# Kernel optimization log

Hardware: AMD Instinct MI355X
Metric: run time of the kernel (lower is better)

## Reference

```python
import jax, jax.numpy as jnp
import numpy as np

NUM_CLUSTERS = 256
NUM_HEADS = 16
DIM_PER_HEAD = 64
NGRAM_VOCAB = 768 * 256
NGRAM_EMB_DIM = 8
DECAY = 0.999
EPS_PQ = 1e-06
LN_EPS = 1e-05


def _first_primes_after(start, count):
    primes = []
    n = start
    while len(primes) < count:
        n += 1
        if all(n % p for p in range(2, int(n ** 0.5) + 1)):
            primes.append(n)
    return np.array(primes, dtype=np.int64)

# first NUM_HEADS primes in (NGRAM_VOCAB, 2*NGRAM_VOCAB), matching sympy.primerange
_PRIMES = _first_primes_after(NGRAM_VOCAB, NUM_HEADS)


def _layer_norm(v, scale, bias):
    # reduction over last axis; per-(head, feature) scale/bias (flax feature_axes=(-2,-1))
    mu = jnp.mean(v, axis=-1, keepdims=True)
    var = jnp.var(v, axis=-1, keepdims=True)
    return (v - mu) * jax.lax.rsqrt(var + LN_EPS) * scale + bias


def setup_inputs() -> dict:
    key = jax.random.key(0)
    k1, k2, k3 = jax.random.split(key, 3)
    B, L = 4, 4096
    x = jax.random.normal(k1, (B, L, NUM_HEADS * DIM_PER_HEAD), dtype=jnp.float32)
    means = jax.random.normal(k2, (NUM_HEADS, NUM_CLUSTERS, DIM_PER_HEAD), dtype=jnp.float32)
    embed_table = jax.random.normal(k3, (NGRAM_VOCAB * NUM_HEADS, NGRAM_EMB_DIM), dtype=jnp.float32)
    ln_x_scale = jnp.ones((NUM_HEADS, DIM_PER_HEAD), dtype=jnp.float32)
    ln_x_bias = jnp.zeros((NUM_HEADS, DIM_PER_HEAD), dtype=jnp.float32)
    ln_y_scale = jnp.ones((NUM_HEADS, NGRAM_EMB_DIM), dtype=jnp.float32)
    ln_y_bias = jnp.zeros((NUM_HEADS, NGRAM_EMB_DIM), dtype=jnp.float32)
    return {"x": x, "means": means, "embed_table": embed_table,
            "ln_x_scale": ln_x_scale, "ln_x_bias": ln_x_bias,
            "ln_y_scale": ln_y_scale, "ln_y_bias": ln_y_bias}


def reference(x, means, embed_table, ln_x_scale, ln_x_bias, ln_y_scale, ln_y_bias):
    B, L, HD = x.shape
    H, K, D = means.shape
    E = NGRAM_EMB_DIM
    xh = x.reshape(B, L, H, D)

    # --- ProductQuantization: squared-distance cluster assignment ---
    x_sq = jnp.sum(jnp.square(xh), axis=-1, keepdims=True)            # [B,L,H,1]
    m_sq = jnp.sum(jnp.square(means), axis=-1)[None, None]            # [1,1,H,K]
    dists = x_sq + m_sq - 2.0 * jnp.einsum('blhd,hkd->blhk', xh, means)
    cluster_ids = jnp.argmin(dists, axis=-1).astype(jnp.int32)        # [B,L,H]

    # --- EMA means update (train-mode side effect) ---
    one_hot = jax.nn.one_hot(cluster_ids, K, dtype=xh.dtype)          # [B,L,H,K]
    counts = jnp.sum(one_hot, axis=(0, 1))                            # [H,K]
    sum_x = jnp.einsum('blhk,blhd->hkd', one_hot, xh)                 # [H,K,D]
    means_x = sum_x / (EPS_PQ + counts[..., None])
    new_means = (1.0 - DECAY) * means_x + DECAY * means

    # --- bigram ids: ids[t] + ids[t-1] * vocab ---
    prev = jnp.pad(cluster_ids[:, :-1], ((0, 0), (1, 0), (0, 0)))     # [B,L,H]
    ngram_cluster_ids = cluster_ids + prev * NUM_CLUSTERS             # < K*K, fits int32

    # --- multi-way hash per head ---
    head = jnp.arange(H, dtype=jnp.int32)                             # [H]
    primes = jnp.asarray(_PRIMES, dtype=jnp.int32)                    # [H]
    hashed = (ngram_cluster_ids * (head + 1) + (head + 1)) % primes % NGRAM_VOCAB
    ngram_ids = hashed + NGRAM_VOCAB * head                           # [B,L,H]

    # --- ngram embedding gather + per-head LayerNorms + concat ---
    y = embed_table[ngram_ids]                                        # [B,L,H,E]
    normed_x = _layer_norm(xh, ln_x_scale, ln_x_bias)
    normed_y = _layer_norm(y, ln_y_scale, ln_y_bias)
    out = jnp.concatenate((normed_x[..., : D - E], normed_y), axis=-1)
    out = out.reshape(B, L, H * D)
    return out, new_means
```

## Files before the change

kernel.cpp:

```cpp
#include <hip/hip_runtime.h>
#include <cstdint>
#include <cstddef>

#define NH 16
#define ND 64
#define NK 256
#define NE 8
#define NV 196608
#define NBL 16384
#define TOK 64
#define MROW 17
#define ACC_STRIDE 257

struct Primes { int p[NH]; };

__global__ __launch_bounds__(512, 4) void k_pq(
    const float* __restrict__ x, const float* __restrict__ means,
    const float* __restrict__ lnxs, const float* __restrict__ lnxb,
    float* __restrict__ out, uint8_t* __restrict__ cids,
    float* __restrict__ gsum, int* __restrict__ gcnt)
{
  __shared__ __align__(16) float smem[18176];
  float4* sm4   = (float4*)smem;
  float*  smsq2 = smem + 17408;
  int*    scnt  = (int*)(smem + 17920);
  float*  accum = smem;

  const int tid = threadIdx.x;
  const int c   = tid & 31;
  const int r   = tid >> 5;
  const int h   = blockIdx.y;
  const int g0  = blockIdx.x * TOK;

  {
    const int cl = tid & 255, hf = tid >> 8;
    const float4* src = (const float4*)(means + ((size_t)h * NK + cl) * ND + hf * 32);
    float mp = 0.f;
#pragma unroll
    for (int i = 0; i < 8; ++i) {
      float4 v = src[i];
      sm4[cl * MROW + hf * 8 + i] = v;
      mp += v.x * v.x + v.y * v.y + v.z * v.z + v.w * v.w;
    }
    smsq2[hf * NK + cl] = mp;
    if (tid < NK) scnt[tid] = 0;
  }
  __syncthreads();

  float acc[4][8];
#pragma unroll
  for (int j = 0; j < 4; ++j)
#pragma unroll
    for (int i = 0; i < 8; ++i) acc[j][i] = 0.f;

  const float* xb = x + ((size_t)(g0 + r * 4) * NH + h) * ND;

#pragma unroll 2
  for (int dc = 0; dc < 16; ++dc) {
    float4 xv[4];
#pragma unroll
    for (int j = 0; j < 4; ++j)
      xv[j] = *(const float4*)(xb + j * (NH * ND) + dc * 4);
#pragma unroll
    for (int i = 0; i < 8; ++i) {
      float4 mv = sm4[(i * 32 + c) * MROW + dc];
#pragma unroll
      for (int j = 0; j < 4; ++j) {
        float a = acc[j][i];
        a = fmaf(xv[j].x, mv.x, a);
        a = fmaf(xv[j].y, mv.y, a);
        a = fmaf(xv[j].z, mv.z, a);
        a = fmaf(xv[j].w, mv.w, a);
        acc[j][i] = a;
      }
    }
  }

  int bk[4];
  {
    float bv[4]; int bi_[4];
#pragma unroll
    for (int j = 0; j < 4; ++j) { bv[j] = 3.4e38f; bi_[j] = 0; }
#pragma unroll
    for (int i = 0; i < 8; ++i) {
      const int cl = i * 32 + c;
      const float mq = smsq2[cl] + smsq2[NK + cl];
#pragma unroll
      for (int j = 0; j < 4; ++j) {
        float d = mq - 2.0f * acc[j][i];
        if (d < bv[j]) { bv[j] = d; bi_[j] = cl; }
      }
    }
#pragma unroll
    for (int j = 0; j < 4; ++j) {
      float v = bv[j]; int id = bi_[j];
#pragma unroll
      for (int m = 1; m < 32; m <<= 1) {
        float ov = __shfl_xor(v, m);
        int   oi = __shfl_xor(id, m);
        if (ov < v || (ov == v && oi < id)) { v = ov; id = oi; }
      }
      bk[j] = id;
    }
    if (c == 0) {
#pragma unroll
      for (int j = 0; j < 4; ++j) {
        cids[(size_t)(g0 + r * 4 + j) * NH + h] = (uint8_t)bk[j];
        atomicAdd(&scnt[bk[j]], 1);
      }
    }
  }

  __syncthreads();
  for (int idx = tid; idx < ND * ACC_STRIDE; idx += 512) accum[idx] = 0.f;
  __syncthreads();

#pragma unroll
  for (int j = 0; j < 4; ++j) {
    const float* xt = x + ((size_t)(g0 + r * 4 + j) * NH + h) * ND + c * 2;
    float2 v = *(const float2*)xt;
    atomicAdd(&accum[(c * 2 + 0) * ACC_STRIDE + bk[j]], v.x);
    atomicAdd(&accum[(c * 2 + 1) * ACC_STRIDE + bk[j]], v.y);
  }

  {
    const int tl = tid >> 4, q = tid & 15;
#pragma unroll
    for (int rep = 0; rep < 2; ++rep) {
      const int t = tl + rep * 32;
      float4 v = *(const float4*)(x + ((size_t)(g0 + t) * NH + h) * ND + q * 4);
      float s  = v.x + v.y + v.z + v.w;
      float sq = v.x * v.x + v.y * v.y + v.z * v.z + v.w * v.w;
#pragma unroll
      for (int m = 1; m < 16; m <<= 1) { s += __shfl_xor(s, m); sq += __shfl_xor(sq, m); }
      float mu  = s * (1.f / 64.f);
      float var = sq * (1.f / 64.f) - mu * mu;
      float rs  = rsqrtf(var + 1e-5f);
      if (q < 14) {
        float4 sc = *(const float4*)(lnxs + h * ND + q * 4);
        float4 bi = *(const float4*)(lnxb + h * ND + q * 4);
        float4 o;
        o.x = (v.x - mu) * rs * sc.x + bi.x;
        o.y = (v.y - mu) * rs * sc.y + bi.y;
        o.z = (v.z - mu) * rs * sc.z + bi.z;
        o.w = (v.w - mu) * rs * sc.w + bi.w;
        *(float4*)(out + ((size_t)(g0 + t) * NH + h) * ND + q * 4) = o;
      }
    }
  }
  __syncthreads();

  {
    const int cl = tid & 255, dh = tid >> 8;
    const int cnt = scnt[cl];
    if (cnt > 0) {
      if (dh == 0) atomicAdd(&gcnt[h * NK + cl], cnt);
#pragma unroll 4
      for (int d = dh * 32; d < dh * 32 + 32; ++d)
        atomicAdd(&gsum[((size_t)h * ND + d) * NK + cl], accum[d * ACC_STRIDE + cl]);
    }
  }
}

__global__ __launch_bounds__(256) void k_ngram(
    const uint8_t* __restrict__ cids, const float* __restrict__ embed,
    const float* __restrict__ lys, const float* __restrict__ lyb,
    float* __restrict__ out, Primes pr)
{
  const int i = blockIdx.x * 256 + threadIdx.x;
  const int h = i & 15;
  const int g = i >> 4;
  const int l = g & 4095;

  int cid  = (int)cids[i];
  int prev = (l == 0) ? 0 : (int)cids[i - NH];
  int ng   = cid + (prev << 8);
  int hp1  = h + 1;
  int v    = ng * hp1 + hp1;
  const int p = pr.p[h];
  while (v >= p) v -= p;
  if (v >= NV) v -= NV;

  const float4* e4 = (const float4*)(embed + ((size_t)(v + NV * h)) * NE);
  float4 y0 = e4[0], y1 = e4[1];

  float s = ((y0.x + y0.y) + (y0.z + y0.w)) + ((y1.x + y1.y) + (y1.z + y1.w));
  float mu = s * 0.125f;
  float q = y0.x * y0.x + y0.y * y0.y + y0.z * y0.z + y0.w * y0.w
          + y1.x * y1.x + y1.y * y1.y + y1.z * y1.z + y1.w * y1.w;
  float var = q * 0.125f - mu * mu;
  float rs  = rsqrtf(var + 1e-5f);

  const float* sc = lys + h * NE;
  const float* bi = lyb + h * NE;
  float4 o0, o1;
  o0.x = (y0.x - mu) * rs * sc[0] + bi[0];
  o0.y = (y0.y - mu) * rs * sc[1] + bi[1];
  o0.z = (y0.z - mu) * rs * sc[2] + bi[2];
  o0.w = (y0.w - mu) * rs * sc[3] + bi[3];
  o1.x = (y1.x - mu) * rs * sc[4] + bi[4];
  o1.y = (y1.y - mu) * rs * sc[5] + bi[5];
  o1.z = (y1.z - mu) * rs * sc[6] + bi[6];
  o1.w = (y1.w - mu) * rs * sc[7] + bi[7];

  float4* orow = (float4*)(out + ((size_t)g * NH + h) * ND + 56);
  orow[0] = o0;
  orow[1] = o1;
}

__global__ __launch_bounds__(256) void k_means(
    const float* __restrict__ means, const float* __restrict__ gsum,
    const int* __restrict__ gcnt, float* __restrict__ newm)
{
  const int i = blockIdx.x * 256 + threadIdx.x;
  const int d = i & 63;
  const int k = (i >> 6) & 255;
  const int h = i >> 14;
  float cnt = (float)gcnt[h * NK + k];
  float sx  = gsum[((size_t)h * ND + d) * NK + k];
  float mx  = sx / (1e-6f + cnt);
  newm[i] = 0.001f * mx + 0.999f * means[i];
}

extern "C" void kernel_launch(void* const* d_in, const int* in_sizes, int n_in,
                              void* d_out, int out_size, void* d_ws, size_t ws_size,
                              hipStream_t stream)
{
  const float* x     = (const float*)d_in[0];
  const float* means = (const float*)d_in[1];
  const float* embed = (const float*)d_in[2];
  const float* lnxs  = (const float*)d_in[3];
  const float* lnxb  = (const float*)d_in[4];
  const float* lys   = (const float*)d_in[5];
  const float* lyb   = (const float*)d_in[6];

  float* out  = (float*)d_out;
  float* newm = out + (size_t)NBL * NH * ND;

  float*   gsum = (float*)d_ws;
  int*     gcnt = (int*)((char*)d_ws + (size_t)NH * NK * ND * 4);
  uint8_t* cids = (uint8_t*)((char*)d_ws + (size_t)NH * NK * ND * 4 + (size_t)NH * NK * 4);

  hipMemsetAsync(d_ws, 0, (size_t)NH * NK * ND * 4 + (size_t)NH * NK * 4, stream);

  Primes pr;
  {
    int n = NV, c = 0;
    while (c < NH) {
      ++n;
      bool isp = true;
      for (int q = 2; (long long)q * q <= n; ++q)
        if (n % q == 0) { isp = false; break; }
      if (isp) pr.p[c++] = n;
    }
  }

  dim3 g1(NBL / TOK, NH);
  k_pq<<<g1, 512, 0, stream>>>(x, means, lnxs, lnxb, out, cids, gsum, gcnt);
  k_ngram<<<(NBL * NH) / 256, 256, 0, stream>>>(cids, embed, lys, lyb, out, pr);
  k_means<<<(NH * NK * ND) / 256, 256, 0, stream>>>(means, gsum, gcnt, newm);
}
```

Baseline: 336.7 us.

## Double tokens per PQ block, relayout global sums, widen LayerNorm per thread

Each PQ block now handles 128 tokens instead of 64, with every thread computing 8 tokens × 8 clusters. This reuses each shared-memory means load across more FMAs and halves the number of global atomic flushes for sums and counts. The global sum buffer moves to an [h][k][d] layout so the flush atomics write contiguous d addresses and the means-update kernel reads it linearly. The x LayerNorm now gives each thread 16 elements with fewer shuffles. The larger accumulator tile raises register pressure and halves the grid, which may reduce occupancy.

```diff
diff --git a/kernel.cpp b/kernel.cpp
--- a/kernel.cpp
+++ b/kernel.cpp
@@ -8,7 +8,7 @@
 #define NE 8
 #define NV 196608
 #define NBL 16384
-#define TOK 64
+#define TOK 128
 #define MROW 17
 #define ACC_STRIDE 257
 
@@ -47,25 +47,25 @@
   }
   __syncthreads();
 
-  float acc[4][8];
-#pragma unroll
-  for (int j = 0; j < 4; ++j)
+  float acc[8][8];
+#pragma unroll
+  for (int j = 0; j < 8; ++j)
 #pragma unroll
     for (int i = 0; i < 8; ++i) acc[j][i] = 0.f;
 
-  const float* xb = x + ((size_t)(g0 + r * 4) * NH + h) * ND;
+  const float* xb = x + ((size_t)(g0 + r * 8) * NH + h) * ND;
 
 #pragma unroll 2
   for (int dc = 0; dc < 16; ++dc) {
-    float4 xv[4];
-#pragma unroll
-    for (int j = 0; j < 4; ++j)
-      xv[j] = *(const float4*)(xb + j * (NH * ND) + dc * 4);
+    float4 xv[8];
+#pragma unroll
+    for (int j = 0; j < 8; ++j)
+      xv[j] = *(const float4*)(xb + (size_t)j * (NH * ND) + dc * 4);
 #pragma unroll
     for (int i = 0; i < 8; ++i) {
       float4 mv = sm4[(i * 32 + c) * MROW + dc];
 #pragma unroll
-      for (int j = 0; j < 4; ++j) {
+      for (int j = 0; j < 8; ++j) {
         float a = acc[j][i];
         a = fmaf(xv[j].x, mv.x, a);
         a = fmaf(xv[j].y, mv.y, a);
@@ -76,23 +76,23 @@
     }
   }
 
-  int bk[4];
-  {
-    float bv[4]; int bi_[4];
-#pragma unroll
-    for (int j = 0; j < 4; ++j) { bv[j] = 3.4e38f; bi_[j] = 0; }
+  int bk[8];
+  {
+    float bv[8]; int bi_[8];
+#pragma unroll
+    for (int j = 0; j < 8; ++j) { bv[j] = 3.4e38f; bi_[j] = 0; }
 #pragma unroll
     for (int i = 0; i < 8; ++i) {
       const int cl = i * 32 + c;
       const float mq = smsq2[cl] + smsq2[NK + cl];
 #pragma unroll
-      for (int j = 0; j < 4; ++j) {
+      for (int j = 0; j < 8; ++j) {
         float d = mq - 2.0f * acc[j][i];
         if (d < bv[j]) { bv[j] = d; bi_[j] = cl; }
       }
     }
 #pragma unroll
-    for (int j = 0; j < 4; ++j) {
+    for (int j = 0; j < 8; ++j) {
       float v = bv[j]; int id = bi_[j];
 #pragma unroll
       for (int m = 1; m < 32; m <<= 1) {
@@ -104,8 +104,8 @@
     }
     if (c == 0) {
 #pragma unroll
-      for (int j = 0; j < 4; ++j) {
-        cids[(size_t)(g0 + r * 4 + j) * NH + h] = (uint8_t)bk[j];
+      for (int j = 0; j < 8; ++j) {
+        cids[(size_t)(g0 + r * 8 + j) * NH + h] = (uint8_t)bk[j];
         atomicAdd(&scnt[bk[j]], 1);
       }
     }
@@ -116,49 +116,53 @@
   __syncthreads();
 
 #pragma unroll
-  for (int j = 0; j < 4; ++j) {
-    const float* xt = x + ((size_t)(g0 + r * 4 + j) * NH + h) * ND + c * 2;
-    float2 v = *(const float2*)xt;
+  for (int j = 0; j < 8; ++j) {
+    float2 v = *(const float2*)(x + ((size_t)(g0 + r * 8 + j) * NH + h) * ND + c * 2);
     atomicAdd(&accum[(c * 2 + 0) * ACC_STRIDE + bk[j]], v.x);
     atomicAdd(&accum[(c * 2 + 1) * ACC_STRIDE + bk[j]], v.y);
   }
 
   {
-    const int tl = tid >> 4, q = tid & 15;
-#pragma unroll
-    for (int rep = 0; rep < 2; ++rep) {
-      const int t = tl + rep * 32;
-      float4 v = *(const float4*)(x + ((size_t)(g0 + t) * NH + h) * ND + q * 4);
-      float s  = v.x + v.y + v.z + v.w;
-      float sq = v.x * v.x + v.y * v.y + v.z * v.z + v.w * v.w;
-#pragma unroll
-      for (int m = 1; m < 16; m <<= 1) { s += __shfl_xor(s, m); sq += __shfl_xor(sq, m); }
-      float mu  = s * (1.f / 64.f);
-      float var = sq * (1.f / 64.f) - mu * mu;
-      float rs  = rsqrtf(var + 1e-5f);
-      if (q < 14) {
-        float4 sc = *(const float4*)(lnxs + h * ND + q * 4);
-        float4 bi = *(const float4*)(lnxb + h * ND + q * 4);
+    const int tl = tid >> 2, q = tid & 3;
+    const float* xt = x + ((size_t)(g0 + tl) * NH + h) * ND + q * 16;
+    float4 v[4];
+    float s = 0.f, sq = 0.f;
+#pragma unroll
+    for (int j = 0; j < 4; ++j) {
+      v[j] = *(const float4*)(xt + j * 4);
+      s  += v[j].x + v[j].y + v[j].z + v[j].w;
+      sq += v[j].x * v[j].x + v[j].y * v[j].y + v[j].z * v[j].z + v[j].w * v[j].w;
+    }
+    s  += __shfl_xor(s, 1);  sq += __shfl_xor(sq, 1);
+    s  += __shfl_xor(s, 2);  sq += __shfl_xor(sq, 2);
+    float mu  = s * (1.f / 64.f);
+    float var = sq * (1.f / 64.f) - mu * mu;
+    float rs  = rsqrtf(var + 1e-5f);
+    float* orow = out + ((size_t)(g0 + tl) * NH + h) * ND + q * 16;
+#pragma unroll
+    for (int j = 0; j < 4; ++j) {
+      const int d = q * 16 + j * 4;
+      if (d < 56) {
+        float4 sc = *(const float4*)(lnxs + h * ND + d);
+        float4 bi = *(const float4*)(lnxb + h * ND + d);
         float4 o;
-        o.x = (v.x - mu) * rs * sc.x + bi.x;
-        o.y = (v.y - mu) * rs * sc.y + bi.y;
-        o.z = (v.z - mu) * rs * sc.z + bi.z;
-        o.w = (v.w - mu) * rs * sc.w + bi.w;
-        *(float4*)(out + ((size_t)(g0 + t) * NH + h) * ND + q * 4) = o;
-      }
-    }
-  }
-  __syncthreads();
-
-  {
-    const int cl = tid & 255, dh = tid >> 8;
-    const int cnt = scnt[cl];
-    if (cnt > 0) {
-      if (dh == 0) atomicAdd(&gcnt[h * NK + cl], cnt);
-#pragma unroll 4
-      for (int d = dh * 32; d < dh * 32 + 32; ++d)
-        atomicAdd(&gsum[((size_t)h * ND + d) * NK + cl], accum[d * ACC_STRIDE + cl]);
-    }
+        o.x = (v[j].x - mu) * rs * sc.x + bi.x;
+        o.y = (v[j].y - mu) * rs * sc.y + bi.y;
+        o.z = (v[j].z - mu) * rs * sc.z + bi.z;
+        o.w = (v[j].w - mu) * rs * sc.w + bi.w;
+        *(float4*)(orow + j * 4) = o;
+      }
+    }
+  }
+  __syncthreads();
+
+  {
+    const int d = tid & 63, grp = tid >> 6;
+    for (int cl = grp; cl < NK; cl += 8) {
+      if (scnt[cl] > 0)
+        atomicAdd(&gsum[(((size_t)h << 8) + cl) * ND + d], accum[d * ACC_STRIDE + cl]);
+    }
+    if (tid < NK && scnt[tid] > 0) atomicAdd(&gcnt[h * NK + tid], scnt[tid]);
   }
 }
 
@@ -213,12 +217,8 @@
     const int* __restrict__ gcnt, float* __restrict__ newm)
 {
   const int i = blockIdx.x * 256 + threadIdx.x;
-  const int d = i & 63;
-  const int k = (i >> 6) & 255;
-  const int h = i >> 14;
-  float cnt = (float)gcnt[h * NK + k];
-  float sx  = gsum[((size_t)h * ND + d) * NK + k];
-  float mx  = sx / (1e-6f + cnt);
+  float cnt = (float)gcnt[i >> 6];
+  float mx  = gsum[i] / (1e-6f + cnt);
   newm[i] = 0.001f * mx + 0.999f * means[i];
 }
 
```

Result: slower. 450.2 us (+33.7%).

## Compact active clusters, coalesce global sum atomics, prefetch x in PQ kernel

Applied to the files above, without the earlier changes.

Builds a compacted list of clusters that received tokens, then flushes per-cluster sums with one thread per dimension. The global sum buffer changes to [H,K,D] layout so the atomics are contiguous and the means kernel indexes it directly. This replaces the old scattered atomic loop that ran once per cluster over all 256 clusters. It also software-prefetches the next x chunk in the distance loop, reshapes the x LayerNorm to 8 lanes per token, and relaxes launch bounds to 2 waves, which may raise register use at the cost of occupancy.

```diff
diff --git a/kernel.cpp b/kernel.cpp
--- a/kernel.cpp
+++ b/kernel.cpp
@@ -14,17 +14,19 @@
 
 struct Primes { int p[NH]; };
 
-__global__ __launch_bounds__(512, 4) void k_pq(
+__global__ __launch_bounds__(512, 2) void k_pq(
     const float* __restrict__ x, const float* __restrict__ means,
     const float* __restrict__ lnxs, const float* __restrict__ lnxb,
     float* __restrict__ out, uint8_t* __restrict__ cids,
     float* __restrict__ gsum, int* __restrict__ gcnt)
 {
-  __shared__ __align__(16) float smem[18176];
-  float4* sm4   = (float4*)smem;
-  float*  smsq2 = smem + 17408;
-  int*    scnt  = (int*)(smem + 17920);
-  float*  accum = smem;
+  __shared__ __align__(16) float smem[18433];
+  float4* sm4     = (float4*)smem;
+  float*  smsq2   = smem + 17408;
+  int*    scnt    = (int*)(smem + 17920);
+  int*    sactive = (int*)(smem + 18176);
+  int*    snact   = (int*)(smem + 18432);
+  float*  accum   = smem;
 
   const int tid = threadIdx.x;
   const int c   = tid & 31;
@@ -44,6 +46,7 @@
     }
     smsq2[hf * NK + cl] = mp;
     if (tid < NK) scnt[tid] = 0;
+    if (tid == 0) *snact = 0;
   }
   __syncthreads();
 
@@ -55,24 +58,34 @@
 
   const float* xb = x + ((size_t)(g0 + r * 4) * NH + h) * ND;
 
-#pragma unroll 2
+  float4 cur[4];
+#pragma unroll
+  for (int j = 0; j < 4; ++j) cur[j] = *(const float4*)(xb + (size_t)j * (NH * ND));
+
+#pragma unroll 4
   for (int dc = 0; dc < 16; ++dc) {
-    float4 xv[4];
-#pragma unroll
-    for (int j = 0; j < 4; ++j)
-      xv[j] = *(const float4*)(xb + j * (NH * ND) + dc * 4);
+    float4 nxt[4];
+    if (dc + 1 < 16) {
+#pragma unroll
+      for (int j = 0; j < 4; ++j)
+        nxt[j] = *(const float4*)(xb + (size_t)j * (NH * ND) + (dc + 1) * 4);
+    }
 #pragma unroll
     for (int i = 0; i < 8; ++i) {
       float4 mv = sm4[(i * 32 + c) * MROW + dc];
 #pragma unroll
       for (int j = 0; j < 4; ++j) {
         float a = acc[j][i];
-        a = fmaf(xv[j].x, mv.x, a);
-        a = fmaf(xv[j].y, mv.y, a);
-        a = fmaf(xv[j].z, mv.z, a);
-        a = fmaf(xv[j].w, mv.w, a);
+        a = fmaf(cur[j].x, mv.x, a);
+        a = fmaf(cur[j].y, mv.y, a);
+        a = fmaf(cur[j].z, mv.z, a);
+        a = fmaf(cur[j].w, mv.w, a);
         acc[j][i] = a;
       }
+    }
+    if (dc + 1 < 16) {
+#pragma unroll
+      for (int j = 0; j < 4; ++j) cur[j] = nxt[j];
     }
   }
 
@@ -112,52 +125,66 @@
   }
 
   __syncthreads();
+
   for (int idx = tid; idx < ND * ACC_STRIDE; idx += 512) accum[idx] = 0.f;
+  if (tid < NK) {
+    const int cnt = scnt[tid];
+    if (cnt > 0) {
+      int p = atomicAdd(snact, 1);
+      sactive[p] = tid;
+      atomicAdd(&gcnt[h * NK + tid], cnt);
+    }
+  }
   __syncthreads();
 
 #pragma unroll
   for (int j = 0; j < 4; ++j) {
-    const float* xt = x + ((size_t)(g0 + r * 4 + j) * NH + h) * ND + c * 2;
-    float2 v = *(const float2*)xt;
+    float2 v = *(const float2*)(x + ((size_t)(g0 + r * 4 + j) * NH + h) * ND + c * 2);
     atomicAdd(&accum[(c * 2 + 0) * ACC_STRIDE + bk[j]], v.x);
     atomicAdd(&accum[(c * 2 + 1) * ACC_STRIDE + bk[j]], v.y);
   }
 
   {
-    const int tl = tid >> 4, q = tid & 15;
-#pragma unroll
-    for (int rep = 0; rep < 2; ++rep) {
-      const int t = tl + rep * 32;
-      float4 v = *(const float4*)(x + ((size_t)(g0 + t) * NH + h) * ND + q * 4);
-      float s  = v.x + v.y + v.z + v.w;
-      float sq = v.x * v.x + v.y * v.y + v.z * v.z + v.w * v.w;
-#pragma unroll
-      for (int m = 1; m < 16; m <<= 1) { s += __shfl_xor(s, m); sq += __shfl_xor(sq, m); }
-      float mu  = s * (1.f / 64.f);
-      float var = sq * (1.f / 64.f) - mu * mu;
-      float rs  = rsqrtf(var + 1e-5f);
-      if (q < 14) {
-        float4 sc = *(const float4*)(lnxs + h * ND + q * 4);
-        float4 bi = *(const float4*)(lnxb + h * ND + q * 4);
-        float4 o;
-        o.x = (v.x - mu) * rs * sc.x + bi.x;
-        o.y = (v.y - mu) * rs * sc.y + bi.y;
-        o.z = (v.z - mu) * rs * sc.z + bi.z;
-        o.w = (v.w - mu) * rs * sc.w + bi.w;
-        *(float4*)(out + ((size_t)(g0 + t) * NH + h) * ND + q * 4) = o;
-      }
-    }
-  }
-  __syncthreads();
-
-  {
-    const int cl = tid & 255, dh = tid >> 8;
-    const int cnt = scnt[cl];
-    if (cnt > 0) {
-      if (dh == 0) atomicAdd(&gcnt[h * NK + cl], cnt);
-#pragma unroll 4
-      for (int d = dh * 32; d < dh * 32 + 32; ++d)
-        atomicAdd(&gsum[((size_t)h * ND + d) * NK + cl], accum[d * ACC_STRIDE + cl]);
+    const int tl = tid >> 3, q = tid & 7;
+    const float* xt = x + ((size_t)(g0 + tl) * NH + h) * ND + q * 8;
+    float4 v0 = *(const float4*)(xt);
+    float4 v1 = *(const float4*)(xt + 4);
+    float s  = v0.x + v0.y + v0.z + v0.w + v1.x + v1.y + v1.z + v1.w;
+    float sq = v0.x * v0.x + v0.y * v0.y + v0.z * v0.z + v0.w * v0.w
+             + v1.x * v1.x + v1.y * v1.y + v1.z * v1.z + v1.w * v1.w;
+    s  += __shfl_xor(s, 1);  sq += __shfl_xor(sq, 1);
+    s  += __shfl_xor(s, 2);  sq += __shfl_xor(sq, 2);
+    s  += __shfl_xor(s, 4);  sq += __shfl_xor(sq, 4);
+    float mu  = s * (1.f / 64.f);
+    float var = sq * (1.f / 64.f) - mu * mu;
+    float rs  = rsqrtf(var + 1e-5f);
+    if (q < 7) {
+      float4 s0 = *(const float4*)(lnxs + h * ND + q * 8);
+      float4 s1 = *(const float4*)(lnxs + h * ND + q * 8 + 4);
+      float4 b0 = *(const float4*)(lnxb + h * ND + q * 8);
+      float4 b1 = *(const float4*)(lnxb + h * ND + q * 8 + 4);
+      float4 o0, o1;
+      o0.x = (v0.x - mu) * rs * s0.x + b0.x;
+      o0.y = (v0.y - mu) * rs * s0.y + b0.y;
+      o0.z = (v0.z - mu) * rs * s0.z + b0.z;
+      o0.w = (v0.w - mu) * rs * s0.w + b0.w;
+      o1.x = (v1.x - mu) * rs * s1.x + b1.x;
+      o1.y = (v1.y - mu) * rs * s1.y + b1.y;
+      o1.z = (v1.z - mu) * rs * s1.z + b1.z;
+      o1.w = (v1.w - mu) * rs * s1.w + b1.w;
+      float* orow = out + ((size_t)(g0 + tl) * NH + h) * ND + q * 8;
+      *(float4*)(orow)     = o0;
+      *(float4*)(orow + 4) = o1;
+    }
+  }
+  __syncthreads();
+
+  {
+    const int d = tid & 63, grp = tid >> 6;
+    const int nact = *snact;
+    for (int a = grp; a < nact; a += 8) {
+      const int cl = sactive[a];
+      atomicAdd(&gsum[(((size_t)h << 8) + cl) * ND + d], accum[d * ACC_STRIDE + cl]);
     }
   }
 }
@@ -213,12 +240,8 @@
     const int* __restrict__ gcnt, float* __restrict__ newm)
 {
   const int i = blockIdx.x * 256 + threadIdx.x;
-  const int d = i & 63;
-  const int k = (i >> 6) & 255;
-  const int h = i >> 14;
-  float cnt = (float)gcnt[h * NK + k];
-  float sx  = gsum[((size_t)h * ND + d) * NK + k];
-  float mx  = sx / (1e-6f + cnt);
+  float cnt = (float)gcnt[i >> 6];
+  float mx  = gsum[i] / (1e-6f + cnt);
   newm[i] = 0.001f * mx + 0.999f * means[i];
 }
 
```

Result: slower. 369.7 us (+9.8%).
